# Performance work log

Hardware: AMD Instinct MI355X
Metric: run time of the kernel (lower is better)

Reference implementation:

```python
import jax, jax.numpy as jnp
import numpy as np

B, M, S, D, Q, H = 8, 8192, 128, 512, 32, 8
HD = D // H
LN_EPS = 1e-5


def setup_inputs() -> dict:
    key = jax.random.key(0)
    ks = jax.random.split(key, 12)
    inp = {
        "memory": jax.random.normal(ks[0], (B, M, D), dtype=jnp.float32),
        "context": jax.random.normal(ks[1], (B, S, D), dtype=jnp.float32),
        "memory_mask": jax.random.randint(ks[2], (B, M), 0, 2).astype(bool),
        # learned parameters
        "queries_param": jax.random.normal(ks[3], (Q, D), dtype=jnp.float32) * 0.02,
        "ctx_w": jax.random.normal(ks[4], (D, D), dtype=jnp.float32) / np.sqrt(D),
        "ctx_b": jnp.zeros((D,), dtype=jnp.float32),
        "in_w": jax.random.normal(ks[5], (3 * D, D), dtype=jnp.float32) / np.sqrt(D),
        "in_b": jnp.zeros((3 * D,), dtype=jnp.float32),
        "out_w": jax.random.normal(ks[6], (D, D), dtype=jnp.float32) / np.sqrt(D),
        "out_b": jnp.zeros((D,), dtype=jnp.float32),
        "ln_g": jnp.ones((D,), dtype=jnp.float32),
        "ln_b": jnp.zeros((D,), dtype=jnp.float32),
        "gate_w": jax.random.normal(ks[7], (Q, D), dtype=jnp.float32) / np.sqrt(D),
        "gate_b": jnp.zeros((Q,), dtype=jnp.float32),
    }
    return inp


def _forward(memory, context, memory_mask, queries_param, ctx_w, ctx_b,
             in_w, in_b, out_w, out_b, ln_g, ln_b, gate_w, gate_b):
    b = memory.shape[0]
    # pool context over sequence dim (rank-3 path)
    pooled = context.mean(axis=1)  # [B, D]
    # queries + projected context
    queries = queries_param[None, :, :] + (pooled @ ctx_w.T + ctx_b)[:, None, :]  # [B, Q, D]
    # MultiheadAttention in-projection
    wq, wk, wv = in_w[:D], in_w[D:2 * D], in_w[2 * D:]
    bq, bk, bv = in_b[:D], in_b[D:2 * D], in_b[2 * D:]
    qh = (queries @ wq.T + bq).reshape(b, Q, H, HD).transpose(0, 2, 1, 3)   # [B,H,Q,hd]
    kh = (memory @ wk.T + bk).reshape(b, M, H, HD).transpose(0, 2, 1, 3)    # [B,H,M,hd]
    vh = (memory @ wv.T + bv).reshape(b, M, H, HD).transpose(0, 2, 1, 3)    # [B,H,M,hd]
    scale = 1.0 / np.sqrt(HD)
    scores = jnp.einsum('bhqd,bhkd->bhqk', qh * scale, kh)                  # [B,H,Q,M]
    # key_padding_mask: True in memory_mask means valid; invalid -> -inf
    scores = jnp.where(memory_mask[:, None, None, :], scores, -jnp.inf)
    attn = jax.nn.softmax(scores, axis=-1)                                   # [B,H,Q,M]
    ctx_out = jnp.einsum('bhqk,bhkd->bhqd', attn, vh)
    ctx_out = ctx_out.transpose(0, 2, 1, 3).reshape(b, Q, D)
    readouts = ctx_out @ out_w.T + out_b                                     # [B,Q,D]
    attention = attn.mean(axis=1)                                            # [B,Q,M]
    gates = jax.nn.sigmoid(pooled @ gate_w.T + gate_b)                       # [B,Q]
    readouts = readouts * gates[:, :, None]
    mu = readouts.mean(axis=-1, keepdims=True)
    var = readouts.var(axis=-1, keepdims=True)
    readouts_norm = (readouts - mu) * jax.lax.rsqrt(var + LN_EPS) * ln_g + ln_b
    return readouts_norm, attention, gates, queries


def reference(memory, context, memory_mask, queries_param, ctx_w, ctx_b,
              in_w, in_b, out_w, out_b, ln_g, ln_b, gate_w, gate_b):
    return _forward(memory, context, memory_mask, queries_param, ctx_w, ctx_b,
                    in_w, in_b, out_w, out_b, ln_g, ln_b, gate_w, gate_b)
```

## Files before the change

kernel.cpp:

```cpp
#include <hip/hip_runtime.h>
#include <cstdint>

#define BB 8
#define MM 8192
#define SS 128
#define DD 512
#define QQ 32
#define HH 8
#define HDD 64
#define LN_EPS 1e-5f

typedef __bf16 bf16;
typedef _Float16 f16;
typedef __attribute__((ext_vector_type(8))) __bf16 bf16x8;
typedef __attribute__((ext_vector_type(4))) __bf16 bf16x4;
typedef __attribute__((ext_vector_type(8))) _Float16 f16x8;
typedef __attribute__((ext_vector_type(4))) float f32x4;

#define NEG_INF (-__builtin_inff())

__global__ __launch_bounds__(512) void k_front(const float* __restrict__ ctx,
                                               const float* __restrict__ ctx_w,
                                               const float* __restrict__ ctx_b,
                                               const float* __restrict__ qp,
                                               const float* __restrict__ gate_w,
                                               const float* __restrict__ gate_b,
                                               float* __restrict__ q_out,
                                               float* __restrict__ gates_out) {
    __shared__ float pl[DD];
    __shared__ float scratch[512];
    __shared__ float proj[64];
    int blk = blockIdx.x;
    int b = blk >> 3, js = blk & 7;
    int t = threadIdx.x;
    const float* p = ctx + (size_t)b * SS * DD + t;
    float s = 0.f;
#pragma unroll 8
    for (int i = 0; i < SS; i++) s += p[(size_t)i * DD];
    pl[t] = s * (1.0f / SS);
    __syncthreads();
    int r = js * 64 + (t & 63), ks = t >> 6;
    {
        const f32x4* wr = (const f32x4*)(ctx_w + (size_t)r * DD + ks * 64);
        const f32x4* pv = (const f32x4*)(pl + ks * 64);
        float a = 0.f;
#pragma unroll
        for (int k = 0; k < 16; k++) {
            f32x4 w = wr[k], pp = pv[k];
            a += w.x * pp.x + w.y * pp.y + w.z * pp.z + w.w * pp.w;
        }
        scratch[t] = a;
    }
    __syncthreads();
    if (t < 64) {
        float sum = ctx_b[js * 64 + t];
#pragma unroll
        for (int s8 = 0; s8 < 8; s8++) sum += scratch[t + 64 * s8];
        proj[t] = sum;
    }
    __syncthreads();
    int col = js * 64 + (t & 63);
    float pr = proj[t & 63];
#pragma unroll
    for (int qq = 0; qq < 4; qq++) {
        int q = (t >> 6) * 4 + qq;
        q_out[((size_t)(b * QQ + q)) * DD + col] = qp[q * DD + col] + pr;
    }
    if (js == 0 && t < QQ) {
        const f32x4* gw = (const f32x4*)(gate_w + (size_t)t * DD);
        const f32x4* pv = (const f32x4*)pl;
        float ga = 0.f;
#pragma unroll 8
        for (int k = 0; k < DD / 4; k++) {
            f32x4 w = gw[k], pp = pv[k];
            ga += w.x * pp.x + w.y * pp.y + w.z * pp.z + w.w * pp.w;
        }
        gates_out[b * QQ + t] = 1.0f / (1.0f + __expf(-(ga + gate_b[t])));
    }
}

__global__ __launch_bounds__(256) void k_qh(const float* __restrict__ q_in,
                                            const float* __restrict__ in_w,
                                            const float* __restrict__ in_b,
                                            float* __restrict__ qh) {
    __shared__ float qr[QQ * DD];
    int blk = blockIdx.x;
    int b = blk >> 3, js = blk & 7;
    int t = threadIdx.x;
    const f32x4* src = (const f32x4*)(q_in + (size_t)b * QQ * DD);
    f32x4* dst = (f32x4*)qr;
    for (int i = t; i < QQ * DD / 4; i += 256) dst[i] = src[i];
    __syncthreads();
    int j = js * 64 + (t & 63);
    int qg = t >> 6;
    const f32x4* wv = (const f32x4*)(in_w + (size_t)j * DD);
    float acc[8];
#pragma unroll
    for (int e = 0; e < 8; e++) acc[e] = 0.f;
    for (int k = 0; k < DD / 4; k++) {
        f32x4 w = wv[k];
#pragma unroll
        for (int e = 0; e < 8; e++) {
            f32x4 qq = ((const f32x4*)qr)[(qg * 8 + e) * (DD / 4) + k];
            acc[e] += w.x * qq.x + w.y * qq.y + w.z * qq.z + w.w * qq.w;
        }
    }
    float bias = in_b[j];
#pragma unroll
    for (int e = 0; e < 8; e++) {
        int q = qg * 8 + e;
        qh[((size_t)(b * QQ + q)) * DD + j] = 0.125f * (acc[e] + bias);
    }
}

__global__ void k_cvt(const float* __restrict__ src, bf16* __restrict__ dst, int n4) {
    int i = blockIdx.x * blockDim.x + threadIdx.x;
    if (i >= n4) return;
    f32x4 v = ((const f32x4*)src)[i];
    bf16x4 o;
    o.x = (bf16)v.x; o.y = (bf16)v.y; o.z = (bf16)v.z; o.w = (bf16)v.w;
    ((bf16x4*)dst)[i] = o;
}

__global__ __launch_bounds__(256) void k_gemm_kv(const bf16* __restrict__ A,
                                                 const bf16* __restrict__ Bw,
                                                 const float* __restrict__ in_b,
                                                 bf16* __restrict__ kvK,
                                                 bf16* __restrict__ Vt) {
    __shared__ __align__(16) bf16 sm[2 * 128 * 64];
    bf16* As = sm;
    bf16* Bs = sm + 128 * 64;
    int tid = threadIdx.x;
    int w = tid >> 6, l = tid & 63;
    int bid = blockIdx.x;
    int bn = (bid >> 3) & 7;
    int bm = ((bid >> 6) << 3) | (bid & 7);
    int wm = w >> 1, wn = w & 1;
    const f32x4 vzero = {0.f, 0.f, 0.f, 0.f};
    f32x4 acc[4][4];
#pragma unroll
    for (int i = 0; i < 4; i++)
#pragma unroll
        for (int j = 0; j < 4; j++) acc[i][j] = vzero;

    int lr = l >> 3;
    int gc = (l & 7) ^ lr;
    const bf16* Ag = A + (size_t)(bm * 128) * DD;
    const bf16* Bg = Bw + (size_t)(bn * 128) * DD;
    int lq = l & 15, quad = l >> 4, lx = lq & 7;

    for (int k0 = 0; k0 < DD; k0 += 64) {
        __syncthreads();
#pragma unroll
        for (int i = 0; i < 4; i++) {
            int seg = w * 4 + i;
            const bf16* ga = Ag + (size_t)(seg * 8 + lr) * DD + k0 + gc * 8;
            const bf16* gb = Bg + (size_t)(seg * 8 + lr) * DD + k0 + gc * 8;
            __builtin_amdgcn_global_load_lds((const __attribute__((address_space(1))) void*)ga,
                                             (__attribute__((address_space(3))) void*)(As + seg * 512),
                                             16, 0, 0);
            __builtin_amdgcn_global_load_lds((const __attribute__((address_space(1))) void*)gb,
                                             (__attribute__((address_space(3))) void*)(Bs + seg * 512),
                                             16, 0, 0);
        }
        __syncthreads();
#pragma unroll
        for (int kc = 0; kc < 8; kc += 4) {
            int ch = (quad + kc) ^ lx;
            bf16x8 af[4], bfr[4];
#pragma unroll
            for (int i = 0; i < 4; i++)
                af[i] = *(const bf16x8*)(As + (wm * 64 + i * 16 + lq) * 64 + ch * 8);
#pragma unroll
            for (int j = 0; j < 4; j++)
                bfr[j] = *(const bf16x8*)(Bs + (wn * 64 + j * 16 + lq) * 64 + ch * 8);
#pragma unroll
            for (int i = 0; i < 4; i++)
#pragma unroll
                for (int j = 0; j < 4; j++)
                    acc[i][j] = __builtin_amdgcn_mfma_f32_16x16x32_bf16(af[i], bfr[j], acc[i][j], 0, 0, 0);
        }
    }

    __syncthreads();
    bf16* tile = sm;
    if (bn < 4) {
#pragma unroll
        for (int j = 0; j < 4; j++) {
            int col = wn * 64 + j * 16 + lq;
            float bias = in_b[512 + bn * 128 + col];
            int cc = col >> 3, cl = col & 7;
#pragma unroll
            for (int i = 0; i < 4; i++) {
                int rbase = wm * 64 + i * 16 + quad * 4;
#pragma unroll
                for (int t = 0; t < 4; t++) {
                    int row = rbase + t;
                    tile[row * 128 + ((cc ^ (row & 15)) << 3) + cl] = (bf16)(acc[i][j][t] + bias);
                }
            }
        }
        __syncthreads();
        for (int idx = tid; idx < 2048; idx += 256) {
            int row = idx >> 4, ch2 = idx & 15;
            bf16x8 v = *(const bf16x8*)(tile + row * 128 + ((ch2 ^ (row & 15)) << 3));
            *(bf16x8*)(kvK + (size_t)(bm * 128 + row) * 512 + bn * 128 + ch2 * 8) = v;
        }
    } else {
#pragma unroll
        for (int j = 0; j < 4; j++) {
            int col = wn * 64 + j * 16 + lq;
            float bias = in_b[512 + bn * 128 + col];
            int cs = col & 15;
#pragma unroll
            for (int i = 0; i < 4; i++) {
                int rbase = wm * 64 + i * 16 + quad * 4;
#pragma unroll
                for (int t = 0; t < 4; t++) {
                    int row = rbase + t;
                    tile[col * 128 + (((row >> 3) ^ cs) << 3) + (row & 7)] = (bf16)(acc[i][j][t] + bias);
                }
            }
        }
        __syncthreads();
        int b = bm >> 6;
        int m0 = (bm & 63) * 128;
        int hd0 = (bn - 4) * 128;
        for (int idx = tid; idx < 2048; idx += 256) {
            int col = idx >> 4, ch2 = idx & 15;
            bf16x8 v = *(const bf16x8*)(tile + col * 128 + ((ch2 ^ (col & 15)) << 3));
            *(bf16x8*)(Vt + ((size_t)(b * 512 + hd0 + col)) * MM + m0 + ch2 * 8) = v;
        }
    }
}

__global__ __launch_bounds__(256) void k_scores(const float* __restrict__ qh,
                                                const bf16* __restrict__ kvK,
                                                const int* __restrict__ mask,
                                                f16* __restrict__ s16,
                                                float* __restrict__ statsM,
                                                float* __restrict__ statsS) {
    __shared__ __align__(16) f16 tile[QQ * 528];
    __shared__ float smx[QQ][4];
    __shared__ float sse[QQ][4];
    __shared__ float qmax[QQ];
    int blk = blockIdx.x;
    int mt = blk & 15, h = (blk >> 4) & 7, b = blk >> 7;
    int tid = threadIdx.x, w = tid >> 6, l = tid & 63;
    int lq = l & 15, quad = l >> 4;
    int mbase = mt * 512 + w * 128;

    bf16x8 af[2][2];
#pragma unroll
    for (int i = 0; i < 2; i++)
#pragma unroll
        for (int s = 0; s < 2; s++) {
            const float* qp = qh + ((size_t)(b * QQ + i * 16 + lq)) * DD + h * 64 + s * 32 + quad * 8;
            f32x4 q0 = *(const f32x4*)qp;
            f32x4 q1 = *(const f32x4*)(qp + 4);
            bf16x8 v;
            v[0] = (bf16)q0.x; v[1] = (bf16)q0.y; v[2] = (bf16)q0.z; v[3] = (bf16)q0.w;
            v[4] = (bf16)q1.x; v[5] = (bf16)q1.y; v[6] = (bf16)q1.z; v[7] = (bf16)q1.w;
            af[i][s] = v;
        }

    const f32x4 vzero = {0.f, 0.f, 0.f, 0.f};
    f32x4 acc[2][8];
#pragma unroll
    for (int i = 0; i < 2; i++)
#pragma unroll
        for (int n = 0; n < 8; n++) acc[i][n] = vzero;

#pragma unroll
    for (int n = 0; n < 8; n++) {
        int m = mbase + n * 16 + lq;
        const bf16* kp = kvK + ((size_t)(b * MM + m)) * 512 + h * 64 + quad * 8;
        bf16x8 b0 = *(const bf16x8*)kp;
        bf16x8 b1 = *(const bf16x8*)(kp + 32);
#pragma unroll
        for (int i = 0; i < 2; i++) {
            acc[i][n] = __builtin_amdgcn_mfma_f32_16x16x32_bf16(af[i][0], b0, acc[i][n], 0, 0, 0);
            acc[i][n] = __builtin_amdgcn_mfma_f32_16x16x32_bf16(af[i][1], b1, acc[i][n], 0, 0, 0);
        }
    }
#pragma unroll
    for (int n = 0; n < 8; n++) {
        int mv = mask[b * MM + mbase + n * 16 + lq];
        if (!mv) {
#pragma unroll
            for (int i = 0; i < 2; i++)
#pragma unroll
                for (int t = 0; t < 4; t++) acc[i][n][t] = NEG_INF;
        }
    }
    float mx[2][4];
#pragma unroll
    for (int i = 0; i < 2; i++)
#pragma unroll
        for (int t = 0; t < 4; t++) {
            float m = acc[i][0][t];
#pragma unroll
            for (int n = 1; n < 8; n++) m = fmaxf(m, acc[i][n][t]);
            mx[i][t] = m;
        }
#pragma unroll
    for (int off = 1; off < 16; off <<= 1)
#pragma unroll
        for (int i = 0; i < 2; i++)
#pragma unroll
            for (int t = 0; t < 4; t++) mx[i][t] = fmaxf(mx[i][t], __shfl_xor(mx[i][t], off, 64));
    if (lq == 0) {
#pragma unroll
        for (int i = 0; i < 2; i++)
#pragma unroll
            for (int t = 0; t < 4; t++) smx[i * 16 + quad * 4 + t][w] = mx[i][t];
    }
    __syncthreads();
    if (tid < QQ) qmax[tid] = fmaxf(fmaxf(smx[tid][0], smx[tid][1]), fmaxf(smx[tid][2], smx[tid][3]));
    __syncthreads();
    float se[2][4];
#pragma unroll
    for (int i = 0; i < 2; i++)
#pragma unroll
        for (int t = 0; t < 4; t++) {
            float qm = qmax[i * 16 + quad * 4 + t];
            float s = 0.f;
#pragma unroll
            for (int n = 0; n < 8; n++) s += __expf(acc[i][n][t] - qm);
            se[i][t] = s;
        }
#pragma unroll
    for (int off = 1; off < 16; off <<= 1)
#pragma unroll
        for (int i = 0; i < 2; i++)
#pragma unroll
            for (int t = 0; t < 4; t++) se[i][t] += __shfl_xor(se[i][t], off, 64);
    if (lq == 0) {
#pragma unroll
        for (int i = 0; i < 2; i++)
#pragma unroll
            for (int t = 0; t < 4; t++) sse[i * 16 + quad * 4 + t][w] = se[i][t];
    }
#pragma unroll
    for (int n = 0; n < 8; n++) {
        int mloc = w * 128 + n * 16 + lq;
#pragma unroll
        for (int i = 0; i < 2; i++)
#pragma unroll
            for (int t = 0; t < 4; t++)
                tile[(i * 16 + quad * 4 + t) * 528 + mloc] = (f16)acc[i][n][t];
    }
    __syncthreads();
    if (tid < QQ) {
        statsM[(size_t)blk * QQ + tid] = qmax[tid];
        statsS[(size_t)blk * QQ + tid] = sse[tid][0] + sse[tid][1] + sse[tid][2] + sse[tid][3];
    }
    for (int it = tid; it < 2048; it += 256) {
        int q = it >> 6, c = it & 63;
        f16x8 v = *(const f16x8*)(tile + q * 528 + c * 8);
        *(f16x8*)(s16 + ((size_t)((b * HH + h) * QQ + q)) * MM + mt * 512 + c * 8) = v;
    }
}

__global__ __launch_bounds__(256) void k_attn(const f16* __restrict__ s16,
                                              const float* __restrict__ statsM,
                                              const float* __restrict__ statsS,
                                              float* __restrict__ attn_out) {
    __shared__ float cM[128], cS[128], Mh[HH], iLh[HH];
    int blk = blockIdx.x;
    int ms = blk & 3, q = (blk >> 2) & 31, b = blk >> 7;
    int t = threadIdx.x;
    if (t < 128) {
        int h = t >> 4, c = t & 15;
        size_t sidx = (size_t)(((b * HH + h) * 16 + c)) * QQ + q;
        cM[t] = statsM[sidx];
        cS[t] = statsS[sidx];
    }
    __syncthreads();
    if (t < HH) {
        float M = NEG_INF;
#pragma unroll
        for (int c = 0; c < 16; c++) M = fmaxf(M, cM[t * 16 + c]);
        float L = 0.f;
#pragma unroll
        for (int c = 0; c < 16; c++) L += cS[t * 16 + c] * __expf(cM[t * 16 + c] - M);
        Mh[t] = M;
        iLh[t] = (1.0f / L) * (1.0f / HH);
    }
    __syncthreads();
    int m0 = ms * 2048 + t * 8;
    float am[8];
#pragma unroll
    for (int e = 0; e < 8; e++) am[e] = 0.f;
#pragma unroll
    for (int h = 0; h < HH; h++) {
        f16x8 v = *(const f16x8*)(s16 + ((size_t)((b * HH + h) * QQ + q)) * MM + m0);
        float M = Mh[h], iL = iLh[h];
#pragma unroll
        for (int e = 0; e < 8; e++) am[e] += __expf((float)v[e] - M) * iL;
    }
    float* ao = attn_out + (size_t)(b * QQ + q) * MM + m0;
    f32x4 o0 = {am[0], am[1], am[2], am[3]};
    f32x4 o1 = {am[4], am[5], am[6], am[7]};
    *(f32x4*)ao = o0;
    *(f32x4*)(ao + 4) = o1;
}

__global__ __launch_bounds__(256) void k_pv(const f16* __restrict__ s16,
                                            const float* __restrict__ statsM,
                                            const float* __restrict__ statsS,
                                            const bf16* __restrict__ Vt,
                                            float* __restrict__ ctxo_p) {
    __shared__ float ctile[QQ * HDD];
    __shared__ float Mq[QQ], iLq[QQ];
    int blk = blockIdx.x;
    int ck = blk & 7, h = (blk >> 3) & 7, b = blk >> 6;
    int t = threadIdx.x, w = t >> 6, l = t & 63;
    int lq = l & 15, quad = l >> 4;
    if (t < QQ) {
        const float* pM = statsM + (size_t)((b * HH + h) * 16) * QQ + t;
        const float* pS = statsS + (size_t)((b * HH + h) * 16) * QQ + t;
        float M = NEG_INF;
#pragma unroll
        for (int c = 0; c < 16; c++) M = fmaxf(M, pM[c * QQ]);
        float L = 0.f;
#pragma unroll
        for (int c = 0; c < 16; c++) L += pS[c * QQ] * __expf(pM[c * QQ] - M);
        Mq[t] = M;
        iLq[t] = 1.0f / L;
    }
    __syncthreads();
    int m0 = ck * 1024 + w * 256;

    const f16* P0 = s16 + ((size_t)((b * HH + h) * QQ + lq)) * MM + m0 + quad * 8;
    const f16* P1 = P0 + (size_t)16 * MM;
    const bf16* Vrow = Vt + ((size_t)((b * HH + h) * HDD + lq)) * MM + m0 + quad * 8;
    float M0 = Mq[lq], iL0 = iLq[lq];
    float M1 = Mq[16 + lq], iL1 = iLq[16 + lq];

    const f32x4 vzero = {0.f, 0.f, 0.f, 0.f};
    f32x4 acc[2][4];
#pragma unroll
    for (int i = 0; i < 2; i++)
#pragma unroll
        for (int j = 0; j < 4; j++) acc[i][j] = vzero;

#pragma unroll 2
    for (int ks = 0; ks < 256; ks += 32) {
        f16x8 r0 = *(const f16x8*)(P0 + ks);
        f16x8 r1 = *(const f16x8*)(P1 + ks);
        bf16x8 a0, a1;
#pragma unroll
        for (int e = 0; e < 8; e++) a0[e] = (bf16)(__expf((float)r0[e] - M0) * iL0);
#pragma unroll
        for (int e = 0; e < 8; e++) a1[e] = (bf16)(__expf((float)r1[e] - M1) * iL1);
        bf16x8 bv[4];
#pragma unroll
        for (int j = 0; j < 4; j++) bv[j] = *(const bf16x8*)(Vrow + (size_t)j * 16 * MM + ks);
#pragma unroll
        for (int j = 0; j < 4; j++) {
            acc[0][j] = __builtin_amdgcn_mfma_f32_16x16x32_bf16(a0, bv[j], acc[0][j], 0, 0, 0);
            acc[1][j] = __builtin_amdgcn_mfma_f32_16x16x32_bf16(a1, bv[j], acc[1][j], 0, 0, 0);
        }
    }
    for (int i = t; i < QQ * HDD; i += 256) ctile[i] = 0.f;
    __syncthreads();
#pragma unroll
    for (int i = 0; i < 2; i++)
#pragma unroll
        for (int j = 0; j < 4; j++)
#pragma unroll
            for (int tt = 0; tt < 4; tt++) {
                int q = i * 16 + quad * 4 + tt;
                int d = j * 16 + lq;
                atomicAdd(&ctile[q * HDD + d], acc[i][j][tt]);
            }
    __syncthreads();
    float* dst = ctxo_p + (size_t)ck * (BB * QQ * DD);
    for (int i = t; i < QQ * HDD; i += 256) {
        int q = i >> 6, d = i & 63;
        dst[((size_t)(b * QQ + q)) * DD + h * HDD + d] = ctile[i];
    }
}

__global__ __launch_bounds__(256) void k_outln(const float* __restrict__ ctxo_p,
                                               const float* __restrict__ out_w,
                                               const float* __restrict__ out_b,
                                               const float* __restrict__ gates,
                                               const float* __restrict__ ln_g,
                                               const float* __restrict__ ln_b,
                                               float* __restrict__ out0) {
    __shared__ float cr[DD];
    __shared__ float sred[4], sred2[4];
    int bq = blockIdx.x, t = threadIdx.x;
    float c0 = 0.f, c1 = 0.f;
#pragma unroll
    for (int c = 0; c < 8; c++) {
        const float* src = ctxo_p + (size_t)c * (BB * QQ * DD) + (size_t)bq * DD;
        c0 += src[t];
        c1 += src[t + 256];
    }
    cr[t] = c0;
    cr[t + 256] = c1;
    __syncthreads();
    float g = gates[bq];
    const f32x4* cv = (const f32x4*)cr;
    float r[2];
#pragma unroll
    for (int jj = 0; jj < 2; jj++) {
        int j = t + jj * 256;
        const f32x4* wv = (const f32x4*)(out_w + (size_t)j * DD);
        float acc = 0.f;
#pragma unroll 4
        for (int k = 0; k < DD / 4; k++) {
            f32x4 wq = wv[k], cq = cv[k];
            acc += wq.x * cq.x + wq.y * cq.y + wq.z * cq.z + wq.w * cq.w;
        }
        r[jj] = (acc + out_b[j]) * g;
    }
    float s1 = r[0] + r[1];
    float s2 = r[0] * r[0] + r[1] * r[1];
    for (int off = 32; off; off >>= 1) {
        s1 += __shfl_xor(s1, off, 64);
        s2 += __shfl_xor(s2, off, 64);
    }
    int wid = t >> 6;
    if ((t & 63) == 0) { sred[wid] = s1; sred2[wid] = s2; }
    __syncthreads();
    float S1 = sred[0] + sred[1] + sred[2] + sred[3];
    float S2 = sred2[0] + sred2[1] + sred2[2] + sred2[3];
    float mu = S1 * (1.0f / DD);
    float var = S2 * (1.0f / DD) - mu * mu;
    float rs = rsqrtf(var + LN_EPS);
#pragma unroll
    for (int jj = 0; jj < 2; jj++) {
        int j = t + jj * 256;
        out0[(size_t)bq * DD + j] = (r[jj] - mu) * rs * ln_g[j] + ln_b[j];
    }
}

extern "C" void kernel_launch(void* const* d_in, const int* in_sizes, int n_in,
                              void* d_out, int out_size, void* d_ws, size_t ws_size,
                              hipStream_t stream) {
    const float* memory  = (const float*)d_in[0];
    const float* context = (const float*)d_in[1];
    const int*   mask    = (const int*)d_in[2];
    const float* qp      = (const float*)d_in[3];
    const float* ctx_w   = (const float*)d_in[4];
    const float* ctx_b   = (const float*)d_in[5];
    const float* in_w    = (const float*)d_in[6];
    const float* in_b    = (const float*)d_in[7];
    const float* out_w   = (const float*)d_in[8];
    const float* out_b   = (const float*)d_in[9];
    const float* ln_g    = (const float*)d_in[10];
    const float* ln_b    = (const float*)d_in[11];
    const float* gate_w  = (const float*)d_in[12];
    const float* gate_b  = (const float*)d_in[13];

    float* out       = (float*)d_out;
    float* out_ln    = out;
    float* out_attn  = out + 131072;
    float* out_gates = out + 131072 + 2097152;
    float* out_q     = out_gates + 256;

    char* ws = (char*)d_ws;
    bf16*  memB   = (bf16*)ws;
    f16*   s16    = (f16*)ws;
    bf16*  kvK    = (bf16*)(ws + 67108864);
    bf16*  Vt     = (bf16*)(ws + 134217728);
    bf16*  kvwB   = (bf16*)(ws + 201326592);
    float* statsM = (float*)(ws + 201588736);
    float* statsS = (float*)(ws + 201719808);
    float* qh     = (float*)(ws + 202375168);
    float* ctxo_p = (float*)(ws + 202899456);

    k_front<<<64, 512, 0, stream>>>(context, ctx_w, ctx_b, qp, gate_w, gate_b, out_q, out_gates);
    k_qh<<<64, 256, 0, stream>>>(out_q, in_w, in_b, qh);
    k_cvt<<<32768, 256, 0, stream>>>(memory, memB, 8388608);
    k_cvt<<<512, 256, 0, stream>>>(in_w + 262144, kvwB, 131072);
    k_gemm_kv<<<4096, 256, 0, stream>>>(memB, kvwB, in_b, kvK, Vt);
    k_scores<<<1024, 256, 0, stream>>>(qh, kvK, mask, s16, statsM, statsS);
    k_attn<<<1024, 256, 0, stream>>>(s16, statsM, statsS, out_attn);
    k_pv<<<512, 256, 0, stream>>>(s16, statsM, statsS, Vt, ctxo_p);
    k_outln<<<BB * QQ, 256, 0, stream>>>(ctxo_p, out_w, out_b, out_gates, ln_g, ln_b, out_ln);
}
```

Before: 478.0 us.

## Rewrite KV projection GEMM with 256x256 tiles, double-buffered LDS prefetch, head-major K

The K/V projection GEMM moves from 128x128 tiles with 4 waves to 256x256 tiles with 8 waves. It double-buffers LDS loads with split waitcnt barriers, so the next K-slice is fetched while MFMAs run, and raises wave priority around the MFMA blocks. K output is now written head-major [B,H,M,64], which gives contiguous per-head reads in k_scores, and the block index is swizzled for L2 locality. The larger tile needs 128KB of LDS and many more accumulator registers, which may lower occupancy.

```diff
diff --git a/kernel.cpp b/kernel.cpp
--- a/kernel.cpp
+++ b/kernel.cpp
@@ -122,117 +122,185 @@
     ((bf16x4*)dst)[i] = o;
 }
 
-__global__ __launch_bounds__(256) void k_gemm_kv(const bf16* __restrict__ A,
-                                                 const bf16* __restrict__ Bw,
-                                                 const float* __restrict__ in_b,
-                                                 bf16* __restrict__ kvK,
-                                                 bf16* __restrict__ Vt) {
-    __shared__ __align__(16) bf16 sm[2 * 128 * 64];
-    bf16* As = sm;
-    bf16* Bs = sm + 128 * 64;
-    int tid = threadIdx.x;
-    int w = tid >> 6, l = tid & 63;
-    int bid = blockIdx.x;
-    int bn = (bid >> 3) & 7;
-    int bm = ((bid >> 6) << 3) | (bid & 7);
-    int wm = w >> 1, wn = w & 1;
+#define GLOAD(gp, lp)                                                                   \
+    __builtin_amdgcn_global_load_lds((const __attribute__((address_space(1))) void*)(gp), \
+                                     (__attribute__((address_space(3))) void*)(lp), 16, 0, 0)
+
+__global__ __launch_bounds__(512, 2) void k_gemm_kv(const bf16* __restrict__ A,
+                                                    const bf16* __restrict__ Bw,
+                                                    const float* __restrict__ in_b,
+                                                    bf16* __restrict__ Kh,
+                                                    bf16* __restrict__ Vt) {
+    __shared__ __align__(16) bf16 sm[65536];
+    const int tid = threadIdx.x;
+    const int w = tid >> 6, l = tid & 63;
+    const int wm = w >> 2, wn = w & 3;
+    const int lq = l & 15, quad = l >> 4, lx = l & 7;
+    const int lr = l >> 3, gc = (l & 7) ^ lr;
+    const int sb = (w >> 1) * 8 + (w & 1) * 2;
+
+    const int bid = blockIdx.x;
+    const int swz = (bid & 7) * 128 + (bid >> 3);
+    const int bm = swz >> 2, bn = swz & 3;
+
+    const bf16* aPtr = A + (size_t)(bm * 256 + w * 8 + lr) * 512 + gc * 8;
+    const bf16* bPtr = Bw + (size_t)(bn * 256 + sb * 8 + lr) * 512 + gc * 8;
+
+#pragma unroll
+    for (int p = 0; p < 4; p++) GLOAD(aPtr + p * 32768, sm + (p * 8 + w) * 512);
+#pragma unroll
+    for (int p = 0; p < 4; p++) {
+        GLOAD(bPtr + ((p & 1) * 8 + (p >> 1) * 32) * 512,
+              sm + 16384 + (sb + (p & 1) + (p >> 1) * 4) * 512);
+        if (p == 1) __builtin_amdgcn_sched_barrier(0);
+    }
+    aPtr += 64;
+    bPtr += 64;
+
     const f32x4 vzero = {0.f, 0.f, 0.f, 0.f};
-    f32x4 acc[4][4];
-#pragma unroll
-    for (int i = 0; i < 4; i++)
+    f32x4 acc[8][4];
+#pragma unroll
+    for (int i = 0; i < 8; i++)
 #pragma unroll
         for (int j = 0; j < 4; j++) acc[i][j] = vzero;
 
-    int lr = l >> 3;
-    int gc = (l & 7) ^ lr;
-    const bf16* Ag = A + (size_t)(bm * 128) * DD;
-    const bf16* Bg = Bw + (size_t)(bn * 128) * DD;
-    int lq = l & 15, quad = l >> 4, lx = lq & 7;
-
-    for (int k0 = 0; k0 < DD; k0 += 64) {
+#pragma unroll
+    for (int T = 0; T < 8; T++) {
+        bf16* Ab = sm + (T & 1) * 32768;
+        bf16* Bb = Ab + 16384;
+        bf16* AbN = sm + ((T + 1) & 1) * 32768;
+        bf16* BbN = AbN + 16384;
+        const bool pf = (T < 7);
+
+        asm volatile("s_waitcnt vmcnt(2)" ::: "memory");
+        __builtin_amdgcn_s_barrier();
+        bf16x8 af[8][2], b01[2][2];
+        {
+            const int c0 = (quad ^ lx) << 3;
+#pragma unroll
+            for (int i = 0; i < 8; i++) {
+                const bf16* rp = Ab + (wm * 128 + i * 16 + lq) * 64;
+                af[i][0] = *(const bf16x8*)(rp + c0);
+                af[i][1] = *(const bf16x8*)(rp + (c0 ^ 32));
+            }
+#pragma unroll
+            for (int j = 0; j < 2; j++) {
+                const bf16* rp = Bb + (wn * 64 + j * 16 + lq) * 64;
+                b01[j][0] = *(const bf16x8*)(rp + c0);
+                b01[j][1] = *(const bf16x8*)(rp + (c0 ^ 32));
+            }
+        }
+        if (pf) {
+#pragma unroll
+            for (int p = 0; p < 4; p++) GLOAD(aPtr + p * 32768, AbN + (p * 8 + w) * 512);
+            aPtr += 64;
+        }
+        __builtin_amdgcn_s_setprio(1);
+#pragma unroll
+        for (int i = 0; i < 8; i++)
+#pragma unroll
+            for (int j = 0; j < 2; j++) {
+                acc[i][j] = __builtin_amdgcn_mfma_f32_16x16x32_bf16(af[i][0], b01[j][0], acc[i][j], 0, 0, 0);
+                acc[i][j] = __builtin_amdgcn_mfma_f32_16x16x32_bf16(af[i][1], b01[j][1], acc[i][j], 0, 0, 0);
+            }
+        __builtin_amdgcn_s_setprio(0);
+
+        if (pf) {
+            asm volatile("s_waitcnt vmcnt(4)" ::: "memory");
+        } else {
+            asm volatile("s_waitcnt vmcnt(0)" ::: "memory");
+        }
+        __builtin_amdgcn_s_barrier();
+        bf16x8 b23[2][2];
+        {
+            const int c0 = (quad ^ lx) << 3;
+#pragma unroll
+            for (int j = 0; j < 2; j++) {
+                const bf16* rp = Bb + (wn * 64 + 32 + j * 16 + lq) * 64;
+                b23[j][0] = *(const bf16x8*)(rp + c0);
+                b23[j][1] = *(const bf16x8*)(rp + (c0 ^ 32));
+            }
+        }
+        if (pf) {
+#pragma unroll
+            for (int p = 0; p < 4; p++) {
+                GLOAD(bPtr + ((p & 1) * 8 + (p >> 1) * 32) * 512,
+                      BbN + (sb + (p & 1) + (p >> 1) * 4) * 512);
+                if (p == 1) __builtin_amdgcn_sched_barrier(0);
+            }
+            bPtr += 64;
+        }
+        __builtin_amdgcn_s_setprio(1);
+#pragma unroll
+        for (int i = 0; i < 8; i++)
+#pragma unroll
+            for (int j = 0; j < 2; j++) {
+                acc[i][2 + j] = __builtin_amdgcn_mfma_f32_16x16x32_bf16(af[i][0], b23[j][0], acc[i][2 + j], 0, 0, 0);
+                acc[i][2 + j] = __builtin_amdgcn_mfma_f32_16x16x32_bf16(af[i][1], b23[j][1], acc[i][2 + j], 0, 0, 0);
+            }
+        __builtin_amdgcn_s_setprio(0);
+    }
+
+    __syncthreads();
+    const int qn_w = wn >> 1;
+    bf16* qt = sm + (((wm << 1) | qn_w) * 16384);
+    const bool isV = (bn >= 2);
+    if (!isV) {
+#pragma unroll
+        for (int j = 0; j < 4; j++) {
+            int cq = (wn & 1) * 64 + j * 16 + lq;
+            float bias = in_b[512 + bn * 256 + qn_w * 128 + cq];
+            int cc = cq >> 3, cl = cq & 7;
+#pragma unroll
+            for (int i = 0; i < 8; i++) {
+                int rb = i * 16 + quad * 4;
+#pragma unroll
+                for (int t = 0; t < 4; t++) {
+                    int r = rb + t;
+                    qt[r * 128 + (((cc ^ (r & 15)) << 3) | cl)] = (bf16)(acc[i][j][t] + bias);
+                }
+            }
+        }
         __syncthreads();
-#pragma unroll
-        for (int i = 0; i < 4; i++) {
-            int seg = w * 4 + i;
-            const bf16* ga = Ag + (size_t)(seg * 8 + lr) * DD + k0 + gc * 8;
-            const bf16* gb = Bg + (size_t)(seg * 8 + lr) * DD + k0 + gc * 8;
-            __builtin_amdgcn_global_load_lds((const __attribute__((address_space(1))) void*)ga,
-                                             (__attribute__((address_space(3))) void*)(As + seg * 512),
-                                             16, 0, 0);
-            __builtin_amdgcn_global_load_lds((const __attribute__((address_space(1))) void*)gb,
-                                             (__attribute__((address_space(3))) void*)(Bs + seg * 512),
-                                             16, 0, 0);
+        for (int idx = tid; idx < 8192; idx += 512) {
+            int qq2 = idx >> 11;
+            int rr = (idx >> 4) & 127, ch2 = idx & 15;
+            bf16x8 v = *(const bf16x8*)(sm + qq2 * 16384 + rr * 128 + ((ch2 ^ (rr & 15)) << 3));
+            int m = bm * 256 + (qq2 >> 1) * 128 + rr;
+            int cg = bn * 256 + (qq2 & 1) * 128 + ch2 * 8;
+            int b = m >> 13, mloc = m & 8191;
+            int h = cg >> 6, d = cg & 63;
+            *(bf16x8*)(Kh + (((size_t)(b * 8 + h) * 8192 + mloc) << 6) + d) = v;
+        }
+    } else {
+#pragma unroll
+        for (int j = 0; j < 4; j++) {
+            int cq = (wn & 1) * 64 + j * 16 + lq;
+            float bias = in_b[512 + bn * 256 + qn_w * 128 + cq];
+            int cs = cq & 15;
+#pragma unroll
+            for (int i = 0; i < 8; i++) {
+                int rb = i * 16 + quad * 4;
+#pragma unroll
+                for (int t = 0; t < 4; t++) {
+                    int r = rb + t;
+                    qt[cq * 128 + ((((r >> 3) ^ cs) << 3) | (r & 7))] = (bf16)(acc[i][j][t] + bias);
+                }
+            }
         }
         __syncthreads();
-#pragma unroll
-        for (int kc = 0; kc < 8; kc += 4) {
-            int ch = (quad + kc) ^ lx;
-            bf16x8 af[4], bfr[4];
-#pragma unroll
-            for (int i = 0; i < 4; i++)
-                af[i] = *(const bf16x8*)(As + (wm * 64 + i * 16 + lq) * 64 + ch * 8);
-#pragma unroll
-            for (int j = 0; j < 4; j++)
-                bfr[j] = *(const bf16x8*)(Bs + (wn * 64 + j * 16 + lq) * 64 + ch * 8);
-#pragma unroll
-            for (int i = 0; i < 4; i++)
-#pragma unroll
-                for (int j = 0; j < 4; j++)
-                    acc[i][j] = __builtin_amdgcn_mfma_f32_16x16x32_bf16(af[i], bfr[j], acc[i][j], 0, 0, 0);
-        }
-    }
-
-    __syncthreads();
-    bf16* tile = sm;
-    if (bn < 4) {
-#pragma unroll
-        for (int j = 0; j < 4; j++) {
-            int col = wn * 64 + j * 16 + lq;
-            float bias = in_b[512 + bn * 128 + col];
-            int cc = col >> 3, cl = col & 7;
-#pragma unroll
-            for (int i = 0; i < 4; i++) {
-                int rbase = wm * 64 + i * 16 + quad * 4;
-#pragma unroll
-                for (int t = 0; t < 4; t++) {
-                    int row = rbase + t;
-                    tile[row * 128 + ((cc ^ (row & 15)) << 3) + cl] = (bf16)(acc[i][j][t] + bias);
-                }
-            }
-        }
-        __syncthreads();
-        for (int idx = tid; idx < 2048; idx += 256) {
-            int row = idx >> 4, ch2 = idx & 15;
-            bf16x8 v = *(const bf16x8*)(tile + row * 128 + ((ch2 ^ (row & 15)) << 3));
-            *(bf16x8*)(kvK + (size_t)(bm * 128 + row) * 512 + bn * 128 + ch2 * 8) = v;
-        }
-    } else {
-#pragma unroll
-        for (int j = 0; j < 4; j++) {
-            int col = wn * 64 + j * 16 + lq;
-            float bias = in_b[512 + bn * 128 + col];
-            int cs = col & 15;
-#pragma unroll
-            for (int i = 0; i < 4; i++) {
-                int rbase = wm * 64 + i * 16 + quad * 4;
-#pragma unroll
-                for (int t = 0; t < 4; t++) {
-                    int row = rbase + t;
-                    tile[col * 128 + (((row >> 3) ^ cs) << 3) + (row & 7)] = (bf16)(acc[i][j][t] + bias);
-                }
-            }
-        }
-        __syncthreads();
-        int b = bm >> 6;
-        int m0 = (bm & 63) * 128;
-        int hd0 = (bn - 4) * 128;
-        for (int idx = tid; idx < 2048; idx += 256) {
-            int col = idx >> 4, ch2 = idx & 15;
-            bf16x8 v = *(const bf16x8*)(tile + col * 128 + ((ch2 ^ (col & 15)) << 3));
-            *(bf16x8*)(Vt + ((size_t)(b * 512 + hd0 + col)) * MM + m0 + ch2 * 8) = v;
-        }
-    }
-}
+        for (int idx = tid; idx < 8192; idx += 512) {
+            int qq2 = idx >> 11;
+            int cq = (idx >> 4) & 127, ch2 = idx & 15;
+            bf16x8 v = *(const bf16x8*)(sm + qq2 * 16384 + cq * 128 + ((ch2 ^ (cq & 15)) << 3));
+            int hd = (bn - 2) * 256 + (qq2 & 1) * 128 + cq;
+            int m = bm * 256 + (qq2 >> 1) * 128 + ch2 * 8;
+            int b = m >> 13, mloc = m & 8191;
+            *(bf16x8*)(Vt + ((size_t)(b * 512 + hd)) * MM + mloc) = v;
+        }
+    }
+}
+#undef GLOAD
 
 __global__ __launch_bounds__(256) void k_scores(const float* __restrict__ qh,
                                                 const bf16* __restrict__ kvK,
@@ -274,7 +342,7 @@
 #pragma unroll
     for (int n = 0; n < 8; n++) {
         int m = mbase + n * 16 + lq;
-        const bf16* kp = kvK + ((size_t)(b * MM + m)) * 512 + h * 64 + quad * 8;
+        const bf16* kp = kvK + (((size_t)(b * HH + h) * MM + m) << 6) + quad * 8;
         bf16x8 b0 = *(const bf16x8*)kp;
         bf16x8 b1 = *(const bf16x8*)(kp + 32);
 #pragma unroll
@@ -578,7 +646,7 @@
     k_qh<<<64, 256, 0, stream>>>(out_q, in_w, in_b, qh);
     k_cvt<<<32768, 256, 0, stream>>>(memory, memB, 8388608);
     k_cvt<<<512, 256, 0, stream>>>(in_w + 262144, kvwB, 131072);
-    k_gemm_kv<<<4096, 256, 0, stream>>>(memB, kvwB, in_b, kvK, Vt);
+    k_gemm_kv<<<1024, 512, 0, stream>>>(memB, kvwB, in_b, kvK, Vt);
     k_scores<<<1024, 256, 0, stream>>>(qh, kvK, mask, s16, statsM, statsS);
     k_attn<<<1024, 256, 0, stream>>>(s16, statsM, statsS, out_attn);
     k_pv<<<512, 256, 0, stream>>>(s16, statsM, statsS, Vt, ctxo_p);
```

Result: no change. 475.3 us (-0.6%).
